# Kernel tuning notes

Hardware: AMD Instinct MI355X
Metric: run time of the kernel (lower is better)

## Reference

```python
import jax, jax.numpy as jnp
import numpy as np

B, T, D, H = 2, 2048, 1024, 16
HS = D // H  # head_size = 64
DFF = 4 * D


def setup_inputs() -> dict:
    key = jax.random.key(0)
    ks = jax.random.split(key, 12)
    s = 0.02
    return {
        "x": jax.random.normal(ks[0], (B, T, D), dtype=jnp.float32),
        "Wq": jax.random.normal(ks[1], (D, D), dtype=jnp.float32) * s,
        "Wk": jax.random.normal(ks[2], (D, D), dtype=jnp.float32) * s,
        "Wv": jax.random.normal(ks[3], (D, D), dtype=jnp.float32) * s,
        "Wo": jax.random.normal(ks[4], (D, D), dtype=jnp.float32) * s,
        "bo": jnp.zeros((D,), dtype=jnp.float32),
        "W1": jax.random.normal(ks[5], (D, DFF), dtype=jnp.float32) * s,
        "b1": jnp.zeros((DFF,), dtype=jnp.float32),
        "W2": jax.random.normal(ks[6], (DFF, D), dtype=jnp.float32) * s,
        "b2": jnp.zeros((D,), dtype=jnp.float32),
        "g1": jnp.ones((D,), dtype=jnp.float32),
        "be1": jnp.zeros((D,), dtype=jnp.float32),
        "g2": jnp.ones((D,), dtype=jnp.float32),
        "be2": jnp.zeros((D,), dtype=jnp.float32),
    }


def layer_norm(x, g, b, eps=1e-5):
    mu = jnp.mean(x, axis=-1, keepdims=True)
    var = jnp.var(x, axis=-1, keepdims=True)
    return (x - mu) * jax.lax.rsqrt(var + eps) * g + b


def attention(x, Wq, Wk, Wv, Wo, bo):
    # x: [B,T,D] -> q,k,v: [B,H,T,HS]
    def split_heads(y):
        return y.reshape(B, T, H, HS).transpose(0, 2, 1, 3)
    q = split_heads(x @ Wq)
    k = split_heads(x @ Wk)
    v = split_heads(x @ Wv)
    scores = jnp.einsum("bhqd,bhkd->bhqk", q, k) / jnp.sqrt(jnp.float32(HS))
    causal = jnp.tril(jnp.ones((T, T), dtype=bool))
    scores = jnp.where(causal, scores, -jnp.inf)
    probs = jax.nn.softmax(scores, axis=-1)
    out = jnp.einsum("bhqk,bhkd->bhqd", probs, v)
    out = out.transpose(0, 2, 1, 3).reshape(B, T, D)
    return out @ Wo + bo


def reference(x, Wq, Wk, Wv, Wo, bo, W1, b1, W2, b2, g1, be1, g2, be2):
    x = x + attention(layer_norm(x, g1, be1), Wq, Wk, Wv, Wo, bo)
    h = layer_norm(x, g2, be2)
    x = x + (jax.nn.relu(h @ W1 + b1) @ W2 + b2)
    return x
```

## Files before the change

### kernel.cpp

```cpp
#include <hip/hip_runtime.h>
#include <stdint.h>

#define Bc   2
#define Tc   2048
#define Dc   1024
#define Hc   16
#define HSc  64
#define DFFc 4096
#define Mc   (Bc * Tc)

using f32x4 = __attribute__((ext_vector_type(4))) float;
using s16x8 = __attribute__((ext_vector_type(8))) short;

__device__ __forceinline__ ushort f2bf(float f) {
  union { float f; uint32_t u; } v; v.f = f;
  uint32_t r = (v.u + 0x7FFFu + ((v.u >> 16) & 1u)) >> 16;
  return (ushort)r;
}
__device__ __forceinline__ float bf2f(ushort u) {
  union { uint32_t u; float f; } v; v.u = ((uint32_t)u) << 16;
  return v.f;
}
__device__ __forceinline__ uint32_t cvtpk(float a, float b) {
  uint32_t r;
  asm volatile("v_cvt_pk_bf16_f32 %0, %1, %2" : "=v"(r) : "v"(a), "v"(b));
  return r;
}
__device__ __forceinline__ float wredsum(float v) {
#pragma unroll
  for (int o = 32; o > 0; o >>= 1) v += __shfl_down(v, o);
  return v;
}

__device__ __forceinline__ void gload16(const ushort* g, ushort* l) {
  __builtin_amdgcn_global_load_lds(
      (const __attribute__((address_space(1))) void*)g,
      (__attribute__((address_space(3))) void*)l, 16, 0, 0);
}

template <int N> __device__ __forceinline__ void vwait() {
  if constexpr (N == 0) asm volatile("s_waitcnt vmcnt(0)" ::: "memory");
  else if constexpr (N == 3) asm volatile("s_waitcnt vmcnt(3)" ::: "memory");
  else if constexpr (N == 4) asm volatile("s_waitcnt vmcnt(4)" ::: "memory");
  else if constexpr (N == 6) asm volatile("s_waitcnt vmcnt(6)" ::: "memory");
  else asm volatile("s_waitcnt vmcnt(8)" ::: "memory");
}

__global__ __launch_bounds__(256) void tcast_all_kernel(
    const float* __restrict__ Wq, const float* __restrict__ Wk,
    const float* __restrict__ Wv, const float* __restrict__ Wo,
    const float* __restrict__ W1, const float* __restrict__ W2,
    ushort* __restrict__ wqkvt, ushort* __restrict__ wot,
    ushort* __restrict__ w1t, ushort* __restrict__ w2t) {
  __shared__ float t[32][33];
  const int id = blockIdx.x;
  const float* src; ushort* dst; int K, N, bx, by;
  if (id < 4096) {
    const int which = id >> 10, local = id & 1023;
    src = (which == 0) ? Wq : (which == 1) ? Wk : (which == 2) ? Wv : Wo;
    dst = (which == 3) ? wot : wqkvt + (size_t)which * 1024 * 1024;
    K = 1024; N = 1024; bx = local & 31; by = local >> 5;
  } else if (id < 8192) {
    const int local = id - 4096;
    src = W1; dst = w1t; K = 1024; N = 4096;
    bx = local & 127; by = local >> 7;
  } else {
    const int local = id - 8192;
    src = W2; dst = w2t; K = 4096; N = 1024;
    bx = local & 31; by = local >> 5;
  }
  const int tid = threadIdx.x;
  const int n0 = bx * 32, k0 = by * 32;
  const int r = tid >> 3, c4 = (tid & 7) * 4;
  const float4 v = *(const float4*)&src[(size_t)(k0 + r) * N + n0 + c4];
  t[r][c4] = v.x; t[r][c4 + 1] = v.y; t[r][c4 + 2] = v.z; t[r][c4 + 3] = v.w;
  __syncthreads();
  ushort4 o;
  o.x = f2bf(t[c4 + 0][r]); o.y = f2bf(t[c4 + 1][r]);
  o.z = f2bf(t[c4 + 2][r]); o.w = f2bf(t[c4 + 3][r]);
  *(ushort4*)&dst[(size_t)(n0 + r) * K + k0 + c4] = o;
}

__global__ __launch_bounds__(256) void ln_kernel(const float* __restrict__ x,
                                                 const float* __restrict__ g,
                                                 const float* __restrict__ b,
                                                 ushort* __restrict__ out) {
  const int row = blockIdx.x;
  const int tid = threadIdx.x;
  const int lane = tid & 63, wave = tid >> 6;
  const float4 v = ((const float4*)(x + (size_t)row * Dc))[tid];
  float s  = v.x + v.y + v.z + v.w;
  float s2 = v.x * v.x + v.y * v.y + v.z * v.z + v.w * v.w;
  __shared__ float rs[4], rs2[4];
  s = wredsum(s); s2 = wredsum(s2);
  if (lane == 0) { rs[wave] = s; rs2[wave] = s2; }
  __syncthreads();
  const float S  = rs[0] + rs[1] + rs[2] + rs[3];
  const float S2 = rs2[0] + rs2[1] + rs2[2] + rs2[3];
  const float mu = S * (1.f / (float)Dc);
  const float rstd = rsqrtf(S2 * (1.f / (float)Dc) - mu * mu + 1e-5f);
  const float4 gv = ((const float4*)g)[tid];
  const float4 bv = ((const float4*)b)[tid];
  ushort4 o;
  o.x = f2bf((v.x - mu) * rstd * gv.x + bv.x);
  o.y = f2bf((v.y - mu) * rstd * gv.y + bv.y);
  o.z = f2bf((v.z - mu) * rstd * gv.z + bv.z);
  o.w = f2bf((v.w - mu) * rstd * gv.w + bv.w);
  ((ushort4*)(out + (size_t)row * Dc))[tid] = o;
}

template <int BM, int NSPLIT, int OUT_BF16, int RELU, int BIAS, int RES, int QKVSPLIT>
__global__ __launch_bounds__(256) void gemm3_kernel(
    const ushort* __restrict__ A, const ushort* __restrict__ Bt,
    const float* __restrict__ bias, const float* __restrict__ res,
    void* __restrict__ C0, void* __restrict__ C1, void* __restrict__ C2,
    int M, int N, int K) {
  constexpr int MF = BM / 32;
  __shared__ __align__(16) ushort As[BM * 64];
  __shared__ __align__(16) ushort Bs[128 * 64];
  const int tid = threadIdx.x;
  const int lane = tid & 63, w = tid >> 6;
  const int wm = w >> 1, wn = w & 1;
  const int row0 = blockIdx.x * BM, col0 = blockIdx.y * 128;
  const int fr = lane & 15, fg = lane >> 4;
  const int kbeg = (NSPLIT > 1) ? blockIdx.z * (K / NSPLIT) : 0;
  const int kend = (NSPLIT > 1) ? kbeg + K / NSPLIT : K;

  f32x4 acc[MF][4] = {};

  for (int k0 = kbeg; k0 < kend; k0 += 64) {
#pragma unroll
    for (int i = 0; i < BM * 8 / 256; i++) {
      const int c = i * 256 + tid;
      const int r = c >> 3, j = c & 7;
      gload16(A + (size_t)(row0 + r) * K + k0 + ((j ^ (r & 7)) << 3),
              As + (i * 256 + w * 64) * 8);
    }
#pragma unroll
    for (int i = 0; i < 4; i++) {
      const int c = i * 256 + tid;
      const int r = c >> 3, j = c & 7;
      gload16(Bt + (size_t)(col0 + r) * K + k0 + ((j ^ (r & 7)) << 3),
              Bs + (i * 256 + w * 64) * 8);
    }
    __syncthreads();

#pragma unroll
    for (int kk = 0; kk < 2; kk++) {
      const int js = ((kk * 4 + fg) ^ (fr & 7)) << 3;
      s16x8 af[MF], bfr[4];
#pragma unroll
      for (int m = 0; m < MF; m++)
        af[m] = *(const s16x8*)&As[(wm * (BM / 2) + m * 16 + fr) * 64 + js];
#pragma unroll
      for (int n = 0; n < 4; n++)
        bfr[n] = *(const s16x8*)&Bs[(wn * 64 + n * 16 + fr) * 64 + js];
#pragma unroll
      for (int m = 0; m < MF; m++)
#pragma unroll
        for (int n = 0; n < 4; n++)
          acc[m][n] = __builtin_amdgcn_mfma_f32_16x16x32_bf16(af[m], bfr[n], acc[m][n], 0, 0, 0);
    }
    __syncthreads();
  }

  void* Cb = C0;
  int cbase = col0;
  if (QKVSPLIT) {
    const int which = col0 >> 10;
    Cb = (which == 0) ? C0 : (which == 1) ? C1 : C2;
    cbase = col0 & 1023;
  }
  const int NW = QKVSPLIT ? 1024 : N;
#pragma unroll
  for (int m = 0; m < MF; m++) {
#pragma unroll
    for (int n = 0; n < 4; n++) {
#pragma unroll
      for (int i = 0; i < 4; i++) {
        const int r = row0 + wm * (BM / 2) + m * 16 + fg * 4 + i;
        const int c = cbase + wn * 64 + n * 16 + fr;
        float v = acc[m][n][i];
        if (BIAS) v += bias[col0 - cbase + c];
        if (RELU) v = fmaxf(v, 0.f);
        if (RES)  v += res[(size_t)r * NW + c];
        if (OUT_BF16) ((ushort*)Cb)[(size_t)r * NW + c] = f2bf(v);
        else          ((float*)Cb)[(size_t)r * NW + c] = v;
      }
    }
  }
}

template <int BM, int NSPLIT, int OUT_BF16, int RELU, int BIAS, int RES, int QKVSPLIT>
__global__ __launch_bounds__(512, 2) void gemm8_kernel(
    const ushort* __restrict__ A, const ushort* __restrict__ Bt,
    const float* __restrict__ bias, const float* __restrict__ res,
    void* __restrict__ C0, void* __restrict__ C1, void* __restrict__ C2,
    int M, int N, int K) {
  constexpr int WR = BM / 2;
  constexpr int FI = WR / 16;
  constexpr int NPH = FI / 4;
  constexpr int APASS = BM / 128;
  constexpr int LPS = APASS + 2;
  constexpr int SLOT = (BM + 256) * 32;
  __shared__ __align__(16) ushort lds[4 * SLOT];

  const int tid = threadIdx.x;
  const int lane = tid & 63, w = tid >> 6;
  const int wm = w >> 2, wn = w & 3;
  const int fr = lane & 15, fg = lane >> 4;
  const int row0 = blockIdx.x * BM, col0 = blockIdx.y * 256;
  const int kbeg = (NSPLIT > 1) ? blockIdx.z * (K / NSPLIT) : 0;
  const int nt = (K / NSPLIT) / 32;

  const int scc = tid & 3;
  const int sr0 = tid >> 2;

  f32x4 acc[FI][4] = {};

  auto STAGE_A = [&](int t) {
    const int k0 = kbeg + t * 32;
    ushort* base = lds + (size_t)(t & 3) * SLOT;
#pragma unroll
    for (int i = 0; i < APASS; ++i) {
      const int r = i * 128 + sr0;
      const int j = scc ^ ((r >> 1) & 3);
      gload16(A + (size_t)(row0 + r) * K + k0 + j * 8,
              base + (i * 512 + w * 64) * 8);
    }
  };
  auto STAGE_B = [&](int t) {
    const int k0 = kbeg + t * 32;
    ushort* base = lds + (size_t)(t & 3) * SLOT + BM * 32;
#pragma unroll
    for (int i = 0; i < 2; ++i) {
      const int r = i * 128 + sr0;
      const int j = scc ^ ((r >> 1) & 3);
      gload16(Bt + (size_t)(col0 + r) * K + k0 + j * 8,
              base + (i * 512 + w * 64) * 8);
    }
  };

  STAGE_A(0); STAGE_B(0);
  STAGE_A(1); STAGE_B(1);
  STAGE_A(2); STAGE_B(2);
  vwait<2 * LPS>();
  __builtin_amdgcn_sched_barrier(0);
  __builtin_amdgcn_s_barrier();
  __builtin_amdgcn_sched_barrier(0);

  for (int s = 0; s < nt; ++s) {
    const ushort* sb = lds + (size_t)(s & 3) * SLOT;
    s16x8 bf[4];
#pragma unroll
    for (int ni = 0; ni < 4; ++ni) {
      const int rb = wn * 64 + ni * 16 + fr;
      const int ch = fg ^ ((rb >> 1) & 3);
      bf[ni] = *(const s16x8*)&sb[BM * 32 + rb * 32 + ch * 8];
    }
#pragma unroll
    for (int mh = 0; mh < NPH; ++mh) {
      s16x8 af[4];
#pragma unroll
      for (int mi = 0; mi < 4; ++mi) {
        const int ra = wm * WR + mh * 64 + mi * 16 + fr;
        const int ch = fg ^ ((ra >> 1) & 3);
        af[mi] = *(const s16x8*)&sb[ra * 32 + ch * 8];
      }
      if (s + 3 < nt) {
        if constexpr (NPH == 2) {
          if (mh == 0) STAGE_A(s + 3); else STAGE_B(s + 3);
        } else {
          STAGE_A(s + 3); STAGE_B(s + 3);
        }
      }
      __builtin_amdgcn_sched_barrier(0);
      __builtin_amdgcn_s_barrier();
      __builtin_amdgcn_sched_barrier(0);
      __builtin_amdgcn_s_setprio(1);
#pragma unroll
      for (int mi = 0; mi < 4; ++mi)
#pragma unroll
        for (int ni = 0; ni < 4; ++ni)
          acc[mh * 4 + mi][ni] = __builtin_amdgcn_mfma_f32_16x16x32_bf16(
              af[mi], bf[ni], acc[mh * 4 + mi][ni], 0, 0, 0);
      __builtin_amdgcn_s_setprio(0);
      __builtin_amdgcn_sched_barrier(0);
      if (mh == NPH - 1) {
        const int rem = nt - 2 - s;
        if (rem >= 2) vwait<2 * LPS>();
        else if (rem == 1) vwait<LPS>();
        else if (rem == 0) vwait<0>();
      }
      __builtin_amdgcn_s_barrier();
      __builtin_amdgcn_sched_barrier(0);
    }
  }

  __syncthreads();
  if constexpr (NSPLIT > 1 || OUT_BF16) {
    ushort* wst = lds + w * (WR * 64);
#pragma unroll
    for (int mi = 0; mi < FI; ++mi) {
#pragma unroll
      for (int ni = 0; ni < 4; ++ni) {
#pragma unroll
        for (int i = 0; i < 4; ++i) {
          float v = acc[mi][ni][i];
          if (NSPLIT == 1) {
            if (BIAS) v += bias[col0 + wn * 64 + ni * 16 + fr];
            if (RELU) v = fmaxf(v, 0.f);
          }
          wst[(mi * 16 + fg * 4 + i) * 64 + ni * 16 + fr] = f2bf(v);
        }
      }
    }
    const int rr = lane >> 3, cc = (lane & 7) * 8;
    if constexpr (NSPLIT > 1) {
      ushort* P = (ushort*)C0 + (size_t)blockIdx.z * M * N;
#pragma unroll
      for (int it = 0; it < WR / 8; ++it) {
        const int r = it * 8 + rr;
        *(uint4*)&P[(size_t)(row0 + wm * WR + r) * N + col0 + wn * 64 + cc] =
            *(const uint4*)&wst[r * 64 + cc];
      }
    } else {
      void* Cb = C0;
      int cbase = col0;
      if (QKVSPLIT) {
        const int which = col0 >> 10;
        Cb = (which == 0) ? C0 : (which == 1) ? C1 : C2;
        cbase = col0 & 1023;
      }
      const int NW = QKVSPLIT ? 1024 : N;
#pragma unroll
      for (int it = 0; it < WR / 8; ++it) {
        const int r = it * 8 + rr;
        *(uint4*)&((ushort*)Cb)[(size_t)(row0 + wm * WR + r) * NW + cbase + wn * 64 + cc] =
            *(const uint4*)&wst[r * 64 + cc];
      }
    }
  } else {
#pragma unroll
    for (int mi = 0; mi < FI; ++mi)
#pragma unroll
      for (int ni = 0; ni < 4; ++ni)
#pragma unroll
        for (int i = 0; i < 4; ++i) {
          const int r = row0 + wm * WR + mi * 16 + fg * 4 + i;
          const int c = col0 + wn * 64 + ni * 16 + fr;
          float v = acc[mi][ni][i];
          if (BIAS) v += bias[c];
          if (RELU) v = fmaxf(v, 0.f);
          if (RES)  v += res[(size_t)r * N + c];
          ((float*)C0)[(size_t)r * N + c] = v;
        }
  }
}

__global__ __launch_bounds__(256) void sum2b_kernel(const ushort* __restrict__ p,
                                                    const float* __restrict__ bias,
                                                    const float* __restrict__ res,
                                                    float* __restrict__ out) {
  const size_t i = ((size_t)blockIdx.x * 256 + threadIdx.x) * 4;
  const size_t MN = (size_t)Mc * Dc;
  const ushort4 a = *(const ushort4*)(p + i);
  const ushort4 b = *(const ushort4*)(p + MN + i);
  const float4 r = *(const float4*)(res + i);
  const float4 bs = *(const float4*)(bias + (i & 1023));
  float4 o;
  o.x = bf2f(a.x) + bf2f(b.x) + bs.x + r.x;
  o.y = bf2f(a.y) + bf2f(b.y) + bs.y + r.y;
  o.z = bf2f(a.z) + bf2f(b.z) + bs.z + r.z;
  o.w = bf2f(a.w) + bf2f(b.w) + bs.w + r.w;
  *(float4*)(out + i) = o;
}

__global__ __launch_bounds__(512) void fattn3_kernel(const ushort* __restrict__ Q,
                                                     const ushort* __restrict__ K,
                                                     const ushort* __restrict__ V,
                                                     float* __restrict__ pacc,
                                                     float* __restrict__ pl) {
  __shared__ __align__(16) ushort Kl[2][64][72];
  __shared__ __align__(16) ushort Vt[2][64][72];
  __shared__ __align__(16) uint32_t Pu[8][512];

  const int tid = threadIdx.x;
  const int lane = tid & 63, w = tid >> 6;
  const int fr = lane & 15, fg = lane >> 4;

  const int bh   = blockIdx.x & 31;
  const int rest = blockIdx.x >> 5;
  const int qb   = 15 - (rest >> 1);
  const int z    = rest & 1;
  const int h = bh & 15, b = bh >> 4;
  const int q0 = qb * 128;
  const size_t hbase = (size_t)b * Tc * Dc + (size_t)h * HSc;

  s16x8 qf0, qf1;
  {
    const ushort* qp = Q + hbase + (size_t)(q0 + w * 16 + fr) * Dc + fg * 8;
    qf0 = *(const s16x8*)(qp);
    qf1 = *(const s16x8*)(qp + 32);
  }

  const int kkey = tid >> 3, kd8 = (tid & 7) * 8;
  const int vkey = tid & 63, vd8 = (tid >> 6) * 8;

  const int t0 = z * (qb + 1), t1 = (z + 1) * (qb + 1);
  uint4 kreg = *(const uint4*)(K + hbase + (size_t)(t0 * 64 + kkey) * Dc + kd8);
  uint4 vreg = *(const uint4*)(V + hbase + (size_t)(t0 * 64 + vkey) * Dc + vd8);

  f32x4 acc[4] = {};
  float ps = 0.f;
  const float Cs = 0.18033688f;

  for (int kt = t0; kt < t1; kt++) {
    const int cur = (kt - t0) & 1;
    *(uint4*)&Kl[cur][kkey][kd8] = kreg;
    {
      union { uint4 v; ushort u[8]; } t; t.v = vreg;
#pragma unroll
      for (int j = 0; j < 8; j++) Vt[cur][vd8 + j][vkey] = t.u[j];
    }
    if (kt + 1 < t1) {
      kreg = *(const uint4*)(K + hbase + (size_t)((kt + 1) * 64 + kkey) * Dc + kd8);
      vreg = *(const uint4*)(V + hbase + (size_t)((kt + 1) * 64 + vkey) * Dc + vd8);
    }
    __syncthreads();

    const bool skip = (kt * 64 > q0 + w * 16 + 15);
    if (!skip) {
      f32x4 s[4] = {};
      __builtin_amdgcn_s_setprio(1);
#pragma unroll
      for (int kf = 0; kf < 4; kf++) {
        const s16x8 k0 = *(const s16x8*)&Kl[cur][kf * 16 + fr][fg * 8];
        const s16x8 k1 = *(const s16x8*)&Kl[cur][kf * 16 + fr][32 + fg * 8];
        s[kf] = __builtin_amdgcn_mfma_f32_16x16x32_bf16(k0, qf0, s[kf], 0, 0, 0);
        s[kf] = __builtin_amdgcn_mfma_f32_16x16x32_bf16(k1, qf1, s[kf], 0, 0, 0);
      }
      __builtin_amdgcn_s_setprio(0);

      const bool diag = (kt * 64 + 63 > q0 + w * 16);
      const int qg = q0 + w * 16 + fr;
#pragma unroll
      for (int kf = 0; kf < 4; kf++) {
        float p[4];
#pragma unroll
        for (int i = 0; i < 4; i++) {
          p[i] = exp2f(s[kf][i] * Cs);
          if (diag) {
            const int kg = kt * 64 + kf * 16 + fg * 4 + i;
            if (kg > qg) p[i] = 0.f;
          }
          ps += p[i];
        }
        uint2 pk;
        pk.x = cvtpk(p[0], p[1]);
        pk.y = cvtpk(p[2], p[3]);
        *(uint2*)&Pu[w][(2 * kf + (fg >> 1)) * 64 + fr * 4 + (fg & 1) * 2] = pk;
      }

      const s16x8 pa0 = *(const s16x8*)&Pu[w][fg * 64 + fr * 4];
      const s16x8 pa1 = *(const s16x8*)&Pu[w][(4 + fg) * 64 + fr * 4];
      __builtin_amdgcn_s_setprio(1);
#pragma unroll
      for (int df = 0; df < 4; df++) {
        const s16x8 v0 = *(const s16x8*)&Vt[cur][df * 16 + fr][fg * 8];
        const s16x8 v1 = *(const s16x8*)&Vt[cur][df * 16 + fr][32 + fg * 8];
        acc[df] = __builtin_amdgcn_mfma_f32_16x16x32_bf16(pa0, v0, acc[df], 0, 0, 0);
        acc[df] = __builtin_amdgcn_mfma_f32_16x16x32_bf16(pa1, v1, acc[df], 0, 0, 0);
      }
      __builtin_amdgcn_s_setprio(0);
    }
  }

  ps += __shfl_xor(ps, 16);
  ps += __shfl_xor(ps, 32);
  if (lane < 16)
    pl[(size_t)z * (32 * 2048) + (size_t)bh * 2048 + q0 + w * 16 + lane] = ps;

  float* pa = pacc + (size_t)z * (32ull * 2048 * 64) + (size_t)bh * 2048 * 64;
#pragma unroll
  for (int i = 0; i < 4; i++) {
    const int qr = q0 + w * 16 + fg * 4 + i;
#pragma unroll
    for (int df = 0; df < 4; df++)
      pa[(size_t)qr * 64 + df * 16 + fr] = acc[df][i];
  }
}

__global__ __launch_bounds__(256) void amerge_kernel(const float* __restrict__ pacc,
                                                     const float* __restrict__ pl,
                                                     ushort* __restrict__ O) {
  const int g = blockIdx.x * 256 + threadIdx.x;
  const int d4 = g & 15;
  const int t  = (g >> 4) & 2047;
  const int bh = g >> 15;
  const int h = bh & 15, b = bh >> 4;
  const size_t base = ((size_t)bh * 2048 + t) * 64 + d4 * 4;
  const float4 a = *(const float4*)(pacc + base);
  const float4 c = *(const float4*)(pacc + 32ull * 2048 * 64 + base);
  const float inv = 1.f / (pl[(size_t)bh * 2048 + t] + pl[32 * 2048 + (size_t)bh * 2048 + t]);
  ushort4 o;
  o.x = f2bf((a.x + c.x) * inv);
  o.y = f2bf((a.y + c.y) * inv);
  o.z = f2bf((a.z + c.z) * inv);
  o.w = f2bf((a.w + c.w) * inv);
  *(ushort4*)&O[((size_t)(b * 2048 + t)) * 1024 + h * 64 + d4 * 4] = o;
}

extern "C" void kernel_launch(void* const* d_in, const int* in_sizes, int n_in,
                              void* d_out, int out_size, void* d_ws, size_t ws_size,
                              hipStream_t stream) {
  const float* x   = (const float*)d_in[0];
  const float* Wq  = (const float*)d_in[1];
  const float* Wk  = (const float*)d_in[2];
  const float* Wv  = (const float*)d_in[3];
  const float* Wo  = (const float*)d_in[4];
  const float* bo  = (const float*)d_in[5];
  const float* W1  = (const float*)d_in[6];
  const float* b1  = (const float*)d_in[7];
  const float* W2  = (const float*)d_in[8];
  const float* b2  = (const float*)d_in[9];
  const float* g1  = (const float*)d_in[10];
  const float* be1 = (const float*)d_in[11];
  const float* g2  = (const float*)d_in[12];
  const float* be2 = (const float*)d_in[13];

  char* ws = (char*)d_ws;
  const size_t MB = 1ull << 20;
  ushort* ln1   = (ushort*)(ws + 0 * MB);
  ushort* qb    = (ushort*)(ws + 8 * MB);
  ushort* kb    = (ushort*)(ws + 16 * MB);
  ushort* vb    = (ushort*)(ws + 24 * MB);
  ushort* wqkvt = (ushort*)(ws + 32 * MB);
  ushort* wot   = (ushort*)(ws + 38 * MB);
  ushort* w1t   = (ushort*)(ws + 40 * MB);
  ushort* w2t   = (ushort*)(ws + 48 * MB);
  float*  x1    = (float*)(ws + 56 * MB);
  ushort* hb    = (ushort*)(ws + 72 * MB);
  float*  pacc  = (float*)(ws + 56 * MB);
  float*  plv   = (float*)(ws + 88 * MB);
  ushort* fpart = (ushort*)(ws + 0 * MB);

  tcast_all_kernel<<<12288, 256, 0, stream>>>(Wq, Wk, Wv, Wo, W1, W2,
                                              wqkvt, wot, w1t, w2t);

  ln_kernel<<<Mc, 256, 0, stream>>>(x, g1, be1, ln1);

  gemm8_kernel<128, 1, 1, 0, 0, 0, 1><<<dim3(32, 12), 512, 0, stream>>>(
      ln1, wqkvt, nullptr, nullptr, qb, kb, vb, Mc, 3072, Dc);

  fattn3_kernel<<<1024, 512, 0, stream>>>(qb, kb, vb, pacc, plv);
  amerge_kernel<<<4096, 256, 0, stream>>>(pacc, plv, ln1);

  gemm3_kernel<64, 1, 0, 0, 1, 1, 0><<<dim3(64, 8), 256, 0, stream>>>(
      ln1, wot, bo, x, x1, nullptr, nullptr, Mc, Dc, Dc);

  ln_kernel<<<Mc, 256, 0, stream>>>(x1, g2, be2, qb);

  gemm8_kernel<256, 1, 1, 1, 1, 0, 0><<<dim3(16, 16), 512, 0, stream>>>(
      qb, w1t, b1, nullptr, hb, nullptr, nullptr, Mc, DFFc, Dc);

  gemm8_kernel<128, 2, 0, 0, 0, 0, 0><<<dim3(32, 4, 2), 512, 0, stream>>>(
      hb, w2t, nullptr, nullptr, fpart, nullptr, nullptr, Mc, Dc, DFFc);
  sum2b_kernel<<<4096, 256, 0, stream>>>(fpart, b2, x1, (float*)d_out);
}
```

Before: 215.4 us.

## Remap GEMM workgroups across XCDs, unroll LDS ring by four, use incremental load pointers

The gemm8 kernel now remaps its linear workgroup id so that consecutive tiles are spread across the 8 XCDs, aiming for better L2 reuse of shared A/B panels. The main loop is unrolled by the 4-slot LDS ring, so slot offsets become compile-time constants. Global load addresses now use precomputed pointers advanced by 32 each stage instead of per-stage index math. The fp32 non-split epilogue path is removed, so every output goes through the bf16 LDS-staged store, which drops the RES handling in this kernel. The remap assumes the workgroup count divides by 8, and the unrolled loop assumes nt is a multiple of 4.

```diff
diff --git a/kernel.cpp b/kernel.cpp
--- a/kernel.cpp
+++ b/kernel.cpp
@@ -199,7 +199,6 @@
     int M, int N, int K) {
   constexpr int WR = BM / 2;
   constexpr int FI = WR / 16;
-  constexpr int NPH = FI / 4;
   constexpr int APASS = BM / 128;
   constexpr int LPS = APASS + 2;
   constexpr int SLOT = (BM + 256) * 32;
@@ -209,71 +208,61 @@
   const int lane = tid & 63, w = tid >> 6;
   const int wm = w >> 2, wn = w & 3;
   const int fr = lane & 15, fg = lane >> 4;
-  const int row0 = blockIdx.x * BM, col0 = blockIdx.y * 256;
+
+  const int GX = gridDim.x;
+  const int nwg = GX * gridDim.y;
+  const int lid = blockIdx.y * GX + blockIdx.x;
+  const int wg = (lid & 7) * (nwg >> 3) + (lid >> 3);
+  const int row0 = (wg % GX) * BM, col0 = (wg / GX) * 256;
+
   const int kbeg = (NSPLIT > 1) ? blockIdx.z * (K / NSPLIT) : 0;
   const int nt = (K / NSPLIT) / 32;
 
   const int scc = tid & 3;
   const int sr0 = tid >> 2;
+  const int jswz = (scc ^ ((sr0 >> 1) & 3)) * 8;
+
+  const ushort* gA = A + (size_t)(row0 + sr0) * K + kbeg + jswz;
+  const ushort* gB = Bt + (size_t)(col0 + sr0) * K + kbeg + jswz;
 
   f32x4 acc[FI][4] = {};
 
-  auto STAGE_A = [&](int t) {
-    const int k0 = kbeg + t * 32;
-    ushort* base = lds + (size_t)(t & 3) * SLOT;
-#pragma unroll
-    for (int i = 0; i < APASS; ++i) {
-      const int r = i * 128 + sr0;
-      const int j = scc ^ ((r >> 1) & 3);
-      gload16(A + (size_t)(row0 + r) * K + k0 + j * 8,
-              base + (i * 512 + w * 64) * 8);
-    }
+  auto STAGE = [&](int slot) {
+    ushort* ba = lds + slot * SLOT;
+#pragma unroll
+    for (int i = 0; i < APASS; ++i)
+      gload16(gA + (size_t)(i * 128) * K, ba + (i * 512 + w * 64) * 8);
+    ushort* bb = ba + BM * 32;
+#pragma unroll
+    for (int i = 0; i < 2; ++i)
+      gload16(gB + (size_t)(i * 128) * K, bb + (i * 512 + w * 64) * 8);
+    gA += 32; gB += 32;
   };
-  auto STAGE_B = [&](int t) {
-    const int k0 = kbeg + t * 32;
-    ushort* base = lds + (size_t)(t & 3) * SLOT + BM * 32;
-#pragma unroll
-    for (int i = 0; i < 2; ++i) {
-      const int r = i * 128 + sr0;
-      const int j = scc ^ ((r >> 1) & 3);
-      gload16(Bt + (size_t)(col0 + r) * K + k0 + j * 8,
-              base + (i * 512 + w * 64) * 8);
-    }
-  };
-
-  STAGE_A(0); STAGE_B(0);
-  STAGE_A(1); STAGE_B(1);
-  STAGE_A(2); STAGE_B(2);
+
+  STAGE(0); STAGE(1); STAGE(2);
   vwait<2 * LPS>();
   __builtin_amdgcn_sched_barrier(0);
   __builtin_amdgcn_s_barrier();
   __builtin_amdgcn_sched_barrier(0);
 
-  for (int s = 0; s < nt; ++s) {
-    const ushort* sb = lds + (size_t)(s & 3) * SLOT;
-    s16x8 bf[4];
-#pragma unroll
-    for (int ni = 0; ni < 4; ++ni) {
-      const int rb = wn * 64 + ni * 16 + fr;
-      const int ch = fg ^ ((rb >> 1) & 3);
-      bf[ni] = *(const s16x8*)&sb[BM * 32 + rb * 32 + ch * 8];
-    }
-#pragma unroll
-    for (int mh = 0; mh < NPH; ++mh) {
-      s16x8 af[4];
+  for (int sb = 0; sb < nt; sb += 4) {
+#pragma unroll
+    for (int u = 0; u < 4; ++u) {
+      const int s = sb + u;
+      const ushort* sa = lds + u * SLOT;
+      const ushort* sbp = sa + BM * 32;
+      s16x8 af[4], bf[4];
+#pragma unroll
+      for (int ni = 0; ni < 4; ++ni) {
+        const int rb = wn * 64 + ni * 16 + fr;
+        bf[ni] = *(const s16x8*)&sbp[rb * 32 + (fg ^ ((rb >> 1) & 3)) * 8];
+      }
 #pragma unroll
       for (int mi = 0; mi < 4; ++mi) {
-        const int ra = wm * WR + mh * 64 + mi * 16 + fr;
-        const int ch = fg ^ ((ra >> 1) & 3);
-        af[mi] = *(const s16x8*)&sb[ra * 32 + ch * 8];
-      }
-      if (s + 3 < nt) {
-        if constexpr (NPH == 2) {
-          if (mh == 0) STAGE_A(s + 3); else STAGE_B(s + 3);
-        } else {
-          STAGE_A(s + 3); STAGE_B(s + 3);
-        }
-      }
+        const int ra = wm * WR + mi * 16 + fr;
+        af[mi] = *(const s16x8*)&sa[ra * 32 + (fg ^ ((ra >> 1) & 3)) * 8];
+      }
+      if (s + 3 < nt) STAGE((u + 3) & 3);
       __builtin_amdgcn_sched_barrier(0);
       __builtin_amdgcn_s_barrier();
       __builtin_amdgcn_sched_barrier(0);
@@ -282,11 +271,26 @@
       for (int mi = 0; mi < 4; ++mi)
 #pragma unroll
         for (int ni = 0; ni < 4; ++ni)
-          acc[mh * 4 + mi][ni] = __builtin_amdgcn_mfma_f32_16x16x32_bf16(
-              af[mi], bf[ni], acc[mh * 4 + mi][ni], 0, 0, 0);
+          acc[mi][ni] = __builtin_amdgcn_mfma_f32_16x16x32_bf16(
+              af[mi], bf[ni], acc[mi][ni], 0, 0, 0);
       __builtin_amdgcn_s_setprio(0);
+      if constexpr (FI == 8) {
+#pragma unroll
+        for (int mi = 0; mi < 4; ++mi) {
+          const int ra = wm * WR + 64 + mi * 16 + fr;
+          af[mi] = *(const s16x8*)&sa[ra * 32 + (fg ^ ((ra >> 1) & 3)) * 8];
+        }
+        __builtin_amdgcn_s_setprio(1);
+#pragma unroll
+        for (int mi = 0; mi < 4; ++mi)
+#pragma unroll
+          for (int ni = 0; ni < 4; ++ni)
+            acc[4 + mi][ni] = __builtin_amdgcn_mfma_f32_16x16x32_bf16(
+                af[mi], bf[ni], acc[4 + mi][ni], 0, 0, 0);
+        __builtin_amdgcn_s_setprio(0);
+      }
       __builtin_amdgcn_sched_barrier(0);
-      if (mh == NPH - 1) {
+      {
         const int rem = nt - 2 - s;
         if (rem >= 2) vwait<2 * LPS>();
         else if (rem == 1) vwait<LPS>();
@@ -298,63 +302,46 @@
   }
 
   __syncthreads();
-  if constexpr (NSPLIT > 1 || OUT_BF16) {
-    ushort* wst = lds + w * (WR * 64);
-#pragma unroll
-    for (int mi = 0; mi < FI; ++mi) {
-#pragma unroll
-      for (int ni = 0; ni < 4; ++ni) {
-#pragma unroll
-        for (int i = 0; i < 4; ++i) {
-          float v = acc[mi][ni][i];
-          if (NSPLIT == 1) {
-            if (BIAS) v += bias[col0 + wn * 64 + ni * 16 + fr];
-            if (RELU) v = fmaxf(v, 0.f);
-          }
-          wst[(mi * 16 + fg * 4 + i) * 64 + ni * 16 + fr] = f2bf(v);
+  ushort* wst = lds + w * (WR * 64);
+#pragma unroll
+  for (int mi = 0; mi < FI; ++mi) {
+#pragma unroll
+    for (int ni = 0; ni < 4; ++ni) {
+#pragma unroll
+      for (int i = 0; i < 4; ++i) {
+        float v = acc[mi][ni][i];
+        if (NSPLIT == 1) {
+          if (BIAS) v += bias[col0 + wn * 64 + ni * 16 + fr];
+          if (RELU) v = fmaxf(v, 0.f);
         }
-      }
-    }
-    const int rr = lane >> 3, cc = (lane & 7) * 8;
-    if constexpr (NSPLIT > 1) {
-      ushort* P = (ushort*)C0 + (size_t)blockIdx.z * M * N;
-#pragma unroll
-      for (int it = 0; it < WR / 8; ++it) {
-        const int r = it * 8 + rr;
-        *(uint4*)&P[(size_t)(row0 + wm * WR + r) * N + col0 + wn * 64 + cc] =
-            *(const uint4*)&wst[r * 64 + cc];
-      }
-    } else {
-      void* Cb = C0;
-      int cbase = col0;
-      if (QKVSPLIT) {
-        const int which = col0 >> 10;
-        Cb = (which == 0) ? C0 : (which == 1) ? C1 : C2;
-        cbase = col0 & 1023;
-      }
-      const int NW = QKVSPLIT ? 1024 : N;
-#pragma unroll
-      for (int it = 0; it < WR / 8; ++it) {
-        const int r = it * 8 + rr;
-        *(uint4*)&((ushort*)Cb)[(size_t)(row0 + wm * WR + r) * NW + cbase + wn * 64 + cc] =
-            *(const uint4*)&wst[r * 64 + cc];
-      }
+        wst[(mi * 16 + fg * 4 + i) * 64 + ni * 16 + fr] = f2bf(v);
+      }
+    }
+  }
+  const int rr = lane >> 3, cc = (lane & 7) * 8;
+  if constexpr (NSPLIT > 1) {
+    ushort* P = (ushort*)C0 + (size_t)blockIdx.z * M * N;
+#pragma unroll
+    for (int it = 0; it < WR / 8; ++it) {
+      const int r = it * 8 + rr;
+      *(uint4*)&P[(size_t)(row0 + wm * WR + r) * N + col0 + wn * 64 + cc] =
+          *(const uint4*)&wst[r * 64 + cc];
     }
   } else {
-#pragma unroll
-    for (int mi = 0; mi < FI; ++mi)
-#pragma unroll
-      for (int ni = 0; ni < 4; ++ni)
-#pragma unroll
-        for (int i = 0; i < 4; ++i) {
-          const int r = row0 + wm * WR + mi * 16 + fg * 4 + i;
-          const int c = col0 + wn * 64 + ni * 16 + fr;
-          float v = acc[mi][ni][i];
-          if (BIAS) v += bias[c];
-          if (RELU) v = fmaxf(v, 0.f);
-          if (RES)  v += res[(size_t)r * N + c];
-          ((float*)C0)[(size_t)r * N + c] = v;
-        }
+    void* Cb = C0;
+    int cbase = col0;
+    if (QKVSPLIT) {
+      const int which = col0 >> 10;
+      Cb = (which == 0) ? C0 : (which == 1) ? C1 : C2;
+      cbase = col0 & 1023;
+    }
+    const int NW = QKVSPLIT ? 1024 : N;
+#pragma unroll
+    for (int it = 0; it < WR / 8; ++it) {
+      const int r = it * 8 + rr;
+      *(uint4*)&((ushort*)Cb)[(size_t)(row0 + wm * WR + r) * NW + cbase + wn * 64 + cc] =
+          *(const uint4*)&wst[r * 64 + cc];
+    }
   }
 }
 
```

Result: no change. 214.4 us (-0.4%).
